# Performance work log

Measured on AMD Instinct MI355X. Metric: run time of the kernel, lower is better.

The kernel has to match this reference:

```python
import jax, jax.numpy as jnp
import numpy as np

B, S, D = 4, 2048, 1024
E, K, H = 8, 2, 1408
LB_WEIGHT = 0.01


def setup_inputs() -> dict:
    key = jax.random.key(0)
    ks = jax.random.split(key, 7)
    sc = 0.02
    return {
        "x": jax.random.normal(ks[0], (B, S, D), dtype=jnp.float32),
        "Wr": jax.random.normal(ks[1], (D, E), dtype=jnp.float32) * sc,
        "Wg": jax.random.normal(ks[2], (E, D, H), dtype=jnp.float32) * sc,
        "Wu": jax.random.normal(ks[3], (E, D, H), dtype=jnp.float32) * sc,
        "Wx": jax.random.normal(ks[4], (E, D, H), dtype=jnp.float32) * sc,
        "Wd": jax.random.normal(ks[5], (E, H, D), dtype=jnp.float32) * sc,
        "alpha": jnp.ones((E,), dtype=jnp.float32),
    }


def _moe(x, Wr, Wg, Wu, Wx, Wd, alpha):
    Bv, Sv, Dv = x.shape
    xf = x.reshape(-1, Dv)  # [T, D]
    router_probs = jax.nn.softmax(xf @ Wr, axis=-1)  # [T, E]
    topk_p, topk_i = jax.lax.top_k(router_probs, K)  # [T, K]
    topk_p = topk_p / jnp.sum(topk_p, axis=-1, keepdims=True)
    # dense combine weights [T, E]; zero for non-selected experts
    combine = jnp.sum(topk_p[..., None] * jax.nn.one_hot(topk_i, E, dtype=xf.dtype), axis=1)
    out = jnp.zeros_like(xf)
    for e in range(E):
        gate = xf @ Wg[e]
        up = xf @ Wu[e]
        expand = xf @ Wx[e]
        ga = jax.nn.silu(gate) * up
        ea = jax.nn.silu(expand) * up
        combined = alpha[e] * ga + (1.0 - alpha[e]) * ea
        eo = combined @ Wd[e]  # [T, D]
        out = out + eo * combine[:, e:e + 1]
    # load balancing loss: mse(mean usage, 1/E)
    usage = jnp.mean(router_probs, axis=0)
    lb = LB_WEIGHT * jnp.mean((usage - 1.0 / E) ** 2)
    return out.reshape(Bv, Sv, Dv), lb


def reference(x, Wr, Wg, Wu, Wx, Wd, alpha):
    return _moe(x, Wr, Wg, Wu, Wx, Wd, alpha)
```

## Files before the change

kernel.cpp:

```cpp
#include <hip/hip_runtime.h>
#include <stdint.h>

typedef unsigned short u16;
typedef __attribute__((ext_vector_type(8))) short short8;
typedef __attribute__((ext_vector_type(4))) float floatx4;

#define T_TOK 8192
#define DM 1024
#define NE 8
#define HD 1408
#define LDA 72

__device__ __forceinline__ float bf2f(u16 u) {
  union { float f; uint32_t i; } v; v.i = ((uint32_t)u) << 16; return v.f;
}
__device__ __forceinline__ u16 f2bf(float f) {
  union { float f; uint32_t i; } v; v.f = f;
  uint32_t r = v.i + 0x7fffu + ((v.i >> 16) & 1u);
  return (u16)(r >> 16);
}
__device__ __forceinline__ floatx4 mfma16(short8 a, short8 b, floatx4 c) {
  return __builtin_amdgcn_mfma_f32_16x16x32_bf16(a, b, c, 0, 0, 0);
}

__global__ void detect_k(const u16* __restrict__ xraw, int* __restrict__ flag) {
  int lane = threadIdx.x & 63;
  u16 w = xraw[lane * 2];
  int ex = (w >> 7) & 0xFF;
  bool hit = (ex >= 100 && ex <= 135);
  unsigned long long m = __ballot(hit);
  if (lane == 0) *flag = (__popcll(m) >= 40) ? 1 : 0;
}

__global__ void conv_alpha_k(const void* __restrict__ araw, u16* __restrict__ ab,
                             const int* __restrict__ flag) {
  int f = *flag;
  if (threadIdx.x < NE) {
    ab[threadIdx.x] = f ? ((const u16*)araw)[threadIdx.x]
                        : f2bf(((const float*)araw)[threadIdx.x]);
  }
}

__global__ __launch_bounds__(256) void conv_x_k(const void* __restrict__ xraw,
                                                u16* __restrict__ xb,
                                                const int* __restrict__ flag) {
  if (*flag) return;
  size_t base = ((size_t)blockIdx.x * 256 + threadIdx.x) * 8;
  const float* s = (const float*)xraw + base;
  float4 v0 = *(const float4*)s;
  float4 v1 = *(const float4*)(s + 4);
  ushort4 o0, o1;
  o0.x = f2bf(v0.x); o0.y = f2bf(v0.y); o0.z = f2bf(v0.z); o0.w = f2bf(v0.w);
  o1.x = f2bf(v1.x); o1.y = f2bf(v1.y); o1.z = f2bf(v1.z); o1.w = f2bf(v1.w);
  *(ushort4*)(xb + base) = o0;
  *(ushort4*)(xb + base + 4) = o1;
}

__global__ __launch_bounds__(256) void transpose_k(
    const void* __restrict__ src, u16* __restrict__ dst, int R, int C,
    const u16* __restrict__ alphab, int mode, const int* __restrict__ flag) {
  int e = blockIdx.z;
  if (mode) {
    float a = bf2f(alphab[e]);
    if (mode == 1 && a == 1.0f) return;
    if (mode == 2 && a == 0.0f) return;
  }
  int f = *flag;
  __shared__ u16 tile[64][65];
  u16* d = dst + (size_t)e * R * C;
  int c0 = blockIdx.x * 64, r0 = blockIdx.y * 64;
  int tx = threadIdx.x & 63, ty = threadIdx.x >> 6;
  if (f) {
    const u16* s = (const u16*)src + (size_t)e * R * C;
    for (int i = ty; i < 64; i += 4)
      tile[i][tx] = s[(size_t)(r0 + i) * C + (c0 + tx)];
  } else {
    const float* s = (const float*)src + (size_t)e * R * C;
    for (int i = ty; i < 64; i += 4)
      tile[i][tx] = f2bf(s[(size_t)(r0 + i) * C + (c0 + tx)]);
  }
  __syncthreads();
  for (int i = ty; i < 64; i += 4)
    d[(size_t)(c0 + i) * R + (r0 + tx)] = tile[tx][i];
}

__global__ __launch_bounds__(256) void rdot_k(
    const void* __restrict__ x, const void* __restrict__ Wr,
    float* __restrict__ probs, const int* __restrict__ flag) {
  int wave = threadIdx.x >> 6, lane = threadIdx.x & 63;
  int t = blockIdx.x * 4 + wave;
  int f = *flag;
  float acc[8];
  #pragma unroll
  for (int e = 0; e < 8; e++) acc[e] = 0.0f;
  if (f) {
    const u16* xr = (const u16*)x + (size_t)t * DM;
    const u16* wr = (const u16*)Wr;
    #pragma unroll
    for (int i = 0; i < 16; i++) {
      int d = i * 64 + lane;
      float xv = bf2f(xr[d]);
      uint4 wv = *(const uint4*)(wr + (size_t)d * 8);
      acc[0] += xv * bf2f((u16)(wv.x & 0xffff));
      acc[1] += xv * bf2f((u16)(wv.x >> 16));
      acc[2] += xv * bf2f((u16)(wv.y & 0xffff));
      acc[3] += xv * bf2f((u16)(wv.y >> 16));
      acc[4] += xv * bf2f((u16)(wv.z & 0xffff));
      acc[5] += xv * bf2f((u16)(wv.z >> 16));
      acc[6] += xv * bf2f((u16)(wv.w & 0xffff));
      acc[7] += xv * bf2f((u16)(wv.w >> 16));
    }
  } else {
    const float* xr = (const float*)x + (size_t)t * DM;
    const float* wr = (const float*)Wr;
    #pragma unroll
    for (int i = 0; i < 16; i++) {
      int d = i * 64 + lane;
      float xv = xr[d];
      float4 w0 = *(const float4*)(wr + (size_t)d * 8);
      float4 w1 = *(const float4*)(wr + (size_t)d * 8 + 4);
      acc[0] += xv * w0.x; acc[1] += xv * w0.y;
      acc[2] += xv * w0.z; acc[3] += xv * w0.w;
      acc[4] += xv * w1.x; acc[5] += xv * w1.y;
      acc[6] += xv * w1.z; acc[7] += xv * w1.w;
    }
  }
  #pragma unroll
  for (int e = 0; e < 8; e++) {
    #pragma unroll
    for (int s = 32; s; s >>= 1) acc[e] += __shfl_xor(acc[e], s, 64);
  }
  float mx = acc[0];
  #pragma unroll
  for (int e = 1; e < 8; e++) mx = fmaxf(mx, acc[e]);
  float p[8], sum = 0.0f;
  #pragma unroll
  for (int e = 0; e < 8; e++) { p[e] = __expf(acc[e] - mx); sum += p[e]; }
  float inv = 1.0f / sum;
  if (lane < 8) probs[(size_t)t * 8 + lane] = p[lane] * inv;
}

__global__ __launch_bounds__(256) void build_k(
    const float* __restrict__ probs, int* __restrict__ counts,
    float* __restrict__ usage, int* __restrict__ tok_ids,
    float* __restrict__ tok_w) {
  __shared__ int sCnt[8];
  __shared__ int sBase[8];
  __shared__ float sUse[8];
  int tid = threadIdx.x;
  if (tid < 8) { sCnt[tid] = 0; sUse[tid] = 0.0f; }
  __syncthreads();

  int t = blockIdx.x * 256 + tid;
  float4 p0 = *(const float4*)(probs + (size_t)t * 8);
  float4 p1 = *(const float4*)(probs + (size_t)t * 8 + 4);
  float p[8] = {p0.x, p0.y, p0.z, p0.w, p1.x, p1.y, p1.z, p1.w};

  #pragma unroll
  for (int e = 0; e < 8; e++) {
    float v = p[e];
    #pragma unroll
    for (int s = 32; s; s >>= 1) v += __shfl_xor(v, s, 64);
    if ((tid & 63) == 0) atomicAdd(&sUse[e], v);
  }

  int e0 = 0;
  #pragma unroll
  for (int e = 1; e < 8; e++) if (p[e] > p[e0]) e0 = e;
  int e1 = (e0 == 0) ? 1 : 0;
  #pragma unroll
  for (int e = 0; e < 8; e++) if (e != e0 && p[e] > p[e1]) e1 = e;
  float s2 = 1.0f / (p[e0] + p[e1]);

  int s0 = atomicAdd(&sCnt[e0], 1);
  int s1 = atomicAdd(&sCnt[e1], 1);
  __syncthreads();
  if (tid < 8) {
    sBase[tid] = atomicAdd(&counts[tid], sCnt[tid]);
    atomicAdd(&usage[tid], sUse[tid]);
  }
  __syncthreads();
  int i0 = sBase[e0] + s0;
  tok_ids[e0 * T_TOK + i0] = t; tok_w[e0 * T_TOK + i0] = p[e0] * s2;
  int i1 = sBase[e1] + s1;
  tok_ids[e1 * T_TOK + i1] = t; tok_w[e1 * T_TOK + i1] = p[e1] * s2;
}

__global__ void scan_k(const int* __restrict__ counts, int* __restrict__ offs) {
  if (threadIdx.x == 0) {
    int s = 0;
    for (int e = 0; e < 8; e++) { offs[e] = s; s += counts[e]; }
    offs[8] = s;
  }
}

__global__ __launch_bounds__(256, 2) void stageA_k(
    const void* __restrict__ xraw, const u16* __restrict__ xb,
    const u16* __restrict__ WgT, const u16* __restrict__ WuT,
    const u16* __restrict__ WxT, const u16* __restrict__ alphab,
    const int* __restrict__ counts, const int* __restrict__ offs,
    const int* __restrict__ tok_ids, u16* __restrict__ comb,
    const int* __restrict__ flag) {
  int e = blockIdx.z;
  int cnt = counts[e];
  int m0 = blockIdx.y * 128;
  if (m0 >= cnt) return;
  int h0 = blockIdx.x * 64;
  int rem = cnt - m0;
  const u16* x = (*flag) ? (const u16*)xraw : xb;

  alignas(16) __shared__ u16 sA[128 * LDA];
  alignas(16) __shared__ u16 sG[64 * LDA];
  alignas(16) __shared__ u16 sU[64 * LDA];
  alignas(16) __shared__ u16 sX[64 * LDA];
  __shared__ int sTok[128];

  int tid = threadIdx.x;
  if (tid < 128)
    sTok[tid] = tok_ids[e * T_TOK + ((tid < rem) ? (m0 + tid) : m0)];
  __syncthreads();

  float aE = bf2f(alphab[e]);
  bool needG = (aE != 0.0f);
  bool needX = (aE != 1.0f);

  const u16* wg = WgT + (size_t)e * HD * DM;
  const u16* wu = WuT + (size_t)e * HD * DM;
  const u16* wx = WxT + (size_t)e * HD * DM;

  int lane = tid & 63, wave = tid >> 6;
  int wm = wave & 1, wn = wave >> 1;
  int lr = lane & 15, quad = lane >> 4;

  int rowA[4], segA[4], rowW[2], segW[2];
  #pragma unroll
  for (int i = 0; i < 4; i++) { int f = tid + 256 * i; rowA[i] = f >> 3; segA[i] = f & 7; }
  #pragma unroll
  for (int i = 0; i < 2; i++) { int f = tid + 256 * i; rowW[i] = f >> 3; segW[i] = f & 7; }

  floatx4 accG[4][2], accU[4][2], accX[4][2];
  #pragma unroll
  for (int i = 0; i < 4; i++)
    #pragma unroll
    for (int j = 0; j < 2; j++) {
      accG[i][j] = (floatx4)0.0f; accU[i][j] = (floatx4)0.0f; accX[i][j] = (floatx4)0.0f;
    }

  short8 rA[4], rU[2], rG[2], rX[2];
  #pragma unroll
  for (int i = 0; i < 4; i++)
    rA[i] = *(const short8*)(x + (size_t)sTok[rowA[i]] * DM + segA[i] * 8);
  #pragma unroll
  for (int i = 0; i < 2; i++) {
    size_t go = (size_t)(h0 + rowW[i]) * DM + segW[i] * 8;
    rU[i] = *(const short8*)(wu + go);
    if (needG) rG[i] = *(const short8*)(wg + go);
    if (needX) rX[i] = *(const short8*)(wx + go);
  }

  const int NK = DM / 64;
  for (int kt = 0; kt < NK; kt++) {
    __syncthreads();
    #pragma unroll
    for (int i = 0; i < 4; i++)
      *(short8*)&sA[rowA[i] * LDA + segA[i] * 8] = rA[i];
    #pragma unroll
    for (int i = 0; i < 2; i++) {
      *(short8*)&sU[rowW[i] * LDA + segW[i] * 8] = rU[i];
      if (needG) *(short8*)&sG[rowW[i] * LDA + segW[i] * 8] = rG[i];
      if (needX) *(short8*)&sX[rowW[i] * LDA + segW[i] * 8] = rX[i];
    }
    __syncthreads();
    if (kt + 1 < NK) {
      int k0 = (kt + 1) * 64;
      #pragma unroll
      for (int i = 0; i < 4; i++)
        rA[i] = *(const short8*)(x + (size_t)sTok[rowA[i]] * DM + k0 + segA[i] * 8);
      #pragma unroll
      for (int i = 0; i < 2; i++) {
        size_t go = (size_t)(h0 + rowW[i]) * DM + k0 + segW[i] * 8;
        rU[i] = *(const short8*)(wu + go);
        if (needG) rG[i] = *(const short8*)(wg + go);
        if (needX) rX[i] = *(const short8*)(wx + go);
      }
    }
    #pragma unroll
    for (int kk = 0; kk < 2; kk++) {
      int kb = kk * 32 + quad * 8;
      short8 a[4];
      #pragma unroll
      for (int i = 0; i < 4; i++)
        a[i] = *(const short8*)&sA[(wm * 64 + i * 16 + lr) * LDA + kb];
      #pragma unroll
      for (int j = 0; j < 2; j++) {
        int nb = (wn * 32 + j * 16 + lr) * LDA + kb;
        short8 bu = *(const short8*)&sU[nb];
        #pragma unroll
        for (int i = 0; i < 4; i++) accU[i][j] = mfma16(a[i], bu, accU[i][j]);
        if (needG) {
          short8 bg = *(const short8*)&sG[nb];
          #pragma unroll
          for (int i = 0; i < 4; i++) accG[i][j] = mfma16(a[i], bg, accG[i][j]);
        }
        if (needX) {
          short8 bx = *(const short8*)&sX[nb];
          #pragma unroll
          for (int i = 0; i < 4; i++) accX[i][j] = mfma16(a[i], bx, accX[i][j]);
        }
      }
    }
  }

  float a1 = aE, a2 = 1.0f - aE;
  size_t rbase = (size_t)(offs[e] + m0);
  #pragma unroll
  for (int i = 0; i < 4; i++) {
    #pragma unroll
    for (int r = 0; r < 4; r++) {
      int row = wm * 64 + i * 16 + quad * 4 + r;
      if (row < rem) {
        u16* cp = comb + (rbase + row) * HD + h0 + wn * 32 + lr;
        #pragma unroll
        for (int j = 0; j < 2; j++) {
          float g = accG[i][j][r], u = accU[i][j][r], xx = accX[i][j][r];
          float sg = g / (1.0f + __expf(-g));
          float sx = xx / (1.0f + __expf(-xx));
          cp[j * 16] = f2bf(u * (a1 * sg + a2 * sx));
        }
      }
    }
  }
}

__global__ __launch_bounds__(256, 2) void stageB_k(
    const u16* __restrict__ comb, const u16* __restrict__ WdT,
    const int* __restrict__ counts, const int* __restrict__ offs,
    const int* __restrict__ tok_ids, const float* __restrict__ tok_w,
    float* __restrict__ accb) {
  int e = blockIdx.z;
  int cnt = counts[e];
  int m0 = blockIdx.y * 128;
  if (m0 >= cnt) return;
  int d0 = blockIdx.x * 128;
  int rem = cnt - m0;

  alignas(16) __shared__ u16 sA[128 * LDA];
  alignas(16) __shared__ u16 sB[128 * LDA];
  __shared__ int sTok[128];
  __shared__ float sW[128];

  int tid = threadIdx.x;
  if (tid < 128) {
    bool v = tid < rem;
    sTok[tid] = v ? tok_ids[e * T_TOK + m0 + tid] : 0;
    sW[tid] = v ? tok_w[e * T_TOK + m0 + tid] : 0.0f;
  }
  __syncthreads();

  const u16* ca = comb + (size_t)(offs[e] + m0) * HD;
  const u16* wd = WdT + (size_t)e * DM * HD;

  int lane = tid & 63, wave = tid >> 6;
  int wm = wave & 1, wn = wave >> 1;
  int lr = lane & 15, quad = lane >> 4;

  int rowS[4], segS[4], rowC[4];
  #pragma unroll
  for (int i = 0; i < 4; i++) {
    int f = tid + 256 * i;
    rowS[i] = f >> 3; segS[i] = f & 7;
    rowC[i] = (rowS[i] < rem) ? rowS[i] : 0;
  }

  floatx4 acc[4][4];
  #pragma unroll
  for (int i = 0; i < 4; i++)
    #pragma unroll
    for (int j = 0; j < 4; j++) acc[i][j] = (floatx4)0.0f;

  short8 rAr[4], rBr[4];
  #pragma unroll
  for (int i = 0; i < 4; i++) {
    rAr[i] = *(const short8*)(ca + (size_t)rowC[i] * HD + segS[i] * 8);
    rBr[i] = *(const short8*)(wd + (size_t)(d0 + rowS[i]) * HD + segS[i] * 8);
  }

  const int NK = HD / 64;
  for (int kt = 0; kt < NK; kt++) {
    __syncthreads();
    #pragma unroll
    for (int i = 0; i < 4; i++) {
      *(short8*)&sA[rowS[i] * LDA + segS[i] * 8] = rAr[i];
      *(short8*)&sB[rowS[i] * LDA + segS[i] * 8] = rBr[i];
    }
    __syncthreads();
    if (kt + 1 < NK) {
      int k0 = (kt + 1) * 64;
      #pragma unroll
      for (int i = 0; i < 4; i++) {
        rAr[i] = *(const short8*)(ca + (size_t)rowC[i] * HD + k0 + segS[i] * 8);
        rBr[i] = *(const short8*)(wd + (size_t)(d0 + rowS[i]) * HD + k0 + segS[i] * 8);
      }
    }
    #pragma unroll
    for (int kk = 0; kk < 2; kk++) {
      int kb = kk * 32 + quad * 8;
      short8 a[4];
      #pragma unroll
      for (int i = 0; i < 4; i++)
        a[i] = *(const short8*)&sA[(wm * 64 + i * 16 + lr) * LDA + kb];
      #pragma unroll
      for (int j = 0; j < 4; j++) {
        short8 b = *(const short8*)&sB[(wn * 64 + j * 16 + lr) * LDA + kb];
        #pragma unroll
        for (int i = 0; i < 4; i++) acc[i][j] = mfma16(a[i], b, acc[i][j]);
      }
    }
  }

  #pragma unroll
  for (int i = 0; i < 4; i++) {
    #pragma unroll
    for (int r = 0; r < 4; r++) {
      int row = wm * 64 + i * 16 + quad * 4 + r;
      if (row < rem) {
        int t = sTok[row];
        float w = sW[row];
        float* orow = accb + (size_t)t * DM + d0 + wn * 64 + lr;
        #pragma unroll
        for (int j = 0; j < 4; j++)
          atomicAdd(&orow[j * 16], acc[i][j][r] * w);
      }
    }
  }
}

__global__ __launch_bounds__(256) void finalize_k(
    const float* __restrict__ accb, const float* __restrict__ usage,
    void* __restrict__ out, const int* __restrict__ flag) {
  int f = *flag;
  size_t idx = (size_t)blockIdx.x * 256 + threadIdx.x;
  float4 v = ((const float4*)accb)[idx];
  float lb = 0.0f;
  if (idx == 0) {
    for (int e = 0; e < 8; e++) {
      float d = usage[e] * (1.0f / 8192.0f) - 0.125f;
      lb += d * d;
    }
    lb *= 0.01f * 0.125f;
  }
  if (f) {
    u16* o = (u16*)out;
    ushort4 ov;
    ov.x = f2bf(v.x); ov.y = f2bf(v.y); ov.z = f2bf(v.z); ov.w = f2bf(v.w);
    ((ushort4*)o)[idx] = ov;
    if (idx == 0) o[(size_t)T_TOK * DM] = f2bf(lb);
  } else {
    float* o = (float*)out;
    ((float4*)o)[idx] = v;
    if (idx == 0) o[(size_t)T_TOK * DM] = lb;
  }
}

extern "C" void kernel_launch(void* const* d_in, const int* in_sizes, int n_in,
                              void* d_out, int out_size, void* d_ws, size_t ws_size,
                              hipStream_t stream) {
  const void* x  = d_in[0];
  const void* Wr = d_in[1];
  const void* Wg = d_in[2];
  const void* Wu = d_in[3];
  const void* Wx = d_in[4];
  const void* Wd = d_in[5];
  const void* al = d_in[6];
  char* ws = (char*)d_ws;

  int*   counts  = (int*)(ws + 0);
  float* usage   = (float*)(ws + 32);
  int*   flag    = (int*)(ws + 64);
  float* accb    = (float*)(ws + 128);
  int*   offs    = (int*)(ws + 33554560);
  int*   tok_ids = (int*)(ws + 33554624);
  float* tok_w   = (float*)(ws + 33816768);
  u16*   alphab  = (u16*)(ws + 34078912);
  u16*   xb      = (u16*)(ws + 34078976);
  u16*   comb    = (u16*)(ws + 50856192);
  u16*   WgT     = (u16*)(ws + 96993536);
  u16*   WuT     = (u16*)(ws + 120062208);
  u16*   WdT     = (u16*)(ws + 143130880);
  float* probs   = (float*)(ws + 166199552);
  u16*   WxT     = (u16*)(ws + 166461696);

  hipMemsetAsync(ws, 0, 33554560, stream);

  dim3 b256(256, 1, 1);
  detect_k<<<dim3(1), dim3(64), 0, stream>>>((const u16*)x, flag);
  conv_alpha_k<<<dim3(1), dim3(64), 0, stream>>>(al, alphab, flag);
  conv_x_k<<<dim3(4096), b256, 0, stream>>>(x, xb, flag);
  transpose_k<<<dim3(HD / 64, DM / 64, NE), b256, 0, stream>>>(Wg, WgT, DM, HD, alphab, 2, flag);
  transpose_k<<<dim3(HD / 64, DM / 64, NE), b256, 0, stream>>>(Wu, WuT, DM, HD, alphab, 0, flag);
  transpose_k<<<dim3(HD / 64, DM / 64, NE), b256, 0, stream>>>(Wx, WxT, DM, HD, alphab, 1, flag);
  transpose_k<<<dim3(DM / 64, HD / 64, NE), b256, 0, stream>>>(Wd, WdT, HD, DM, alphab, 0, flag);
  rdot_k<<<dim3(T_TOK / 4), b256, 0, stream>>>(x, Wr, probs, flag);
  build_k<<<dim3(T_TOK / 256), b256, 0, stream>>>(probs, counts, usage, tok_ids, tok_w);
  scan_k<<<dim3(1), dim3(64), 0, stream>>>(counts, offs);
  stageA_k<<<dim3(HD / 64, T_TOK / 128, NE), b256, 0, stream>>>(
      x, xb, WgT, WuT, WxT, alphab, counts, offs, tok_ids, comb, flag);
  stageB_k<<<dim3(DM / 128, T_TOK / 128, NE), b256, 0, stream>>>(
      comb, WdT, counts, offs, tok_ids, tok_w, accb);
  finalize_k<<<dim3((T_TOK * DM / 4) / 256), b256, 0, stream>>>(accb, usage, d_out, flag);
}
```

Measured before the change: 520.7 us.

## Add alpha==1 specialized stage-A kernel with direct global-to-LDS loads and wider tiles

Adds a stageA2 kernel for experts with alpha==1 that computes only the gate and up GEMMs, using 128x128 tiles and global_load_lds to copy straight into unpadded shared memory. The original stageA now handles only alpha!=1 experts. stageB switches to the same direct LDS loads and drops its register prefetch. The transpose store now writes pairs of u16 values. Direct LDS loads avoid the register round trip but remove the previous prefetch overlap, and the unpadded 64-wide LDS rows may cause bank conflicts on the MFMA operand reads.

```diff
diff --git a/kernel.cpp b/kernel.cpp
--- a/kernel.cpp
+++ b/kernel.cpp
@@ -18,6 +18,10 @@
   union { float f; uint32_t i; } v; v.f = f;
   uint32_t r = v.i + 0x7fffu + ((v.i >> 16) & 1u);
   return (u16)(r >> 16);
+}
+__device__ __forceinline__ void llds16(const void* g, void* l) {
+  __builtin_amdgcn_global_load_lds((const __attribute__((address_space(1))) void*)g,
+                                   (__attribute__((address_space(3))) void*)l, 16, 0, 0);
 }
 __device__ __forceinline__ floatx4 mfma16(short8 a, short8 b, floatx4 c) {
   return __builtin_amdgcn_mfma_f32_16x16x32_bf16(a, b, c, 0, 0, 0);
@@ -80,8 +84,11 @@
       tile[i][tx] = f2bf(s[(size_t)(r0 + i) * C + (c0 + tx)]);
   }
   __syncthreads();
-  for (int i = ty; i < 64; i += 4)
-    d[(size_t)(c0 + i) * R + (r0 + tx)] = tile[tx][i];
+  int i2 = threadIdx.x >> 5, tx2 = threadIdx.x & 31;
+  for (int ii = i2; ii < 64; ii += 8) {
+    ushort2 v; v.x = tile[2 * tx2][ii]; v.y = tile[2 * tx2 + 1][ii];
+    *(ushort2*)&d[(size_t)(c0 + ii) * R + r0 + 2 * tx2] = v;
+  }
 }
 
 __global__ __launch_bounds__(256) void rdot_k(
@@ -194,6 +201,106 @@
   }
 }
 
+__global__ __launch_bounds__(256, 2) void stageA2_k(
+    const void* __restrict__ xraw, const u16* __restrict__ xb,
+    const u16* __restrict__ WgT, const u16* __restrict__ WuT,
+    const u16* __restrict__ alphab, const int* __restrict__ counts,
+    const int* __restrict__ offs, const int* __restrict__ tok_ids,
+    u16* __restrict__ comb, const int* __restrict__ flag) {
+  int e = blockIdx.z;
+  float aE = bf2f(alphab[e]);
+  if (aE != 1.0f) return;
+  int cnt = counts[e];
+  int m0 = blockIdx.y * 128;
+  if (m0 >= cnt) return;
+  int h0 = blockIdx.x * 128;
+  int rem = cnt - m0;
+  const u16* x = (*flag) ? (const u16*)xraw : xb;
+
+  alignas(16) __shared__ u16 sA[128 * 64];
+  alignas(16) __shared__ u16 sG[128 * 64];
+  alignas(16) __shared__ u16 sU[128 * 64];
+  __shared__ int sTok[128];
+
+  int tid = threadIdx.x;
+  if (tid < 128)
+    sTok[tid] = tok_ids[e * T_TOK + ((tid < rem) ? (m0 + tid) : m0)];
+  __syncthreads();
+
+  const u16* wg = WgT + (size_t)e * HD * DM;
+  const u16* wu = WuT + (size_t)e * HD * DM;
+
+  int lane = tid & 63, wave = tid >> 6;
+  int wm = wave & 1, wn = wave >> 1;
+  int lr = lane & 15, quad = lane >> 4;
+
+  const u16* aptr[4]; const u16* gptr[4]; const u16* uptr[4];
+  u16 *dA[4], *dG[4], *dU[4];
+  #pragma unroll
+  for (int i = 0; i < 4; i++) {
+    int f = tid + 256 * i;
+    int row = f >> 3, seg = f & 7;
+    aptr[i] = x + (size_t)sTok[row] * DM + seg * 8;
+    gptr[i] = wg + (size_t)(h0 + row) * DM + seg * 8;
+    uptr[i] = wu + (size_t)(h0 + row) * DM + seg * 8;
+    dA[i] = &sA[f * 8]; dG[i] = &sG[f * 8]; dU[i] = &sU[f * 8];
+  }
+
+  floatx4 accG[4][4], accU[4][4];
+  #pragma unroll
+  for (int i = 0; i < 4; i++)
+    #pragma unroll
+    for (int j = 0; j < 4; j++) { accG[i][j] = (floatx4)0.0f; accU[i][j] = (floatx4)0.0f; }
+
+  for (int kt = 0; kt < DM / 64; kt++) {
+    int k0 = kt * 64;
+    __syncthreads();
+    #pragma unroll
+    for (int i = 0; i < 4; i++) llds16(aptr[i] + k0, dA[i]);
+    #pragma unroll
+    for (int i = 0; i < 4; i++) llds16(uptr[i] + k0, dU[i]);
+    #pragma unroll
+    for (int i = 0; i < 4; i++) llds16(gptr[i] + k0, dG[i]);
+    __syncthreads();
+    #pragma unroll
+    for (int kk = 0; kk < 2; kk++) {
+      int kb = kk * 32 + quad * 8;
+      short8 a[4];
+      #pragma unroll
+      for (int i = 0; i < 4; i++)
+        a[i] = *(const short8*)&sA[(wm * 64 + i * 16 + lr) * 64 + kb];
+      #pragma unroll
+      for (int j = 0; j < 4; j++) {
+        int nb = (wn * 64 + j * 16 + lr) * 64 + kb;
+        short8 bu = *(const short8*)&sU[nb];
+        #pragma unroll
+        for (int i = 0; i < 4; i++) accU[i][j] = mfma16(a[i], bu, accU[i][j]);
+        short8 bg = *(const short8*)&sG[nb];
+        #pragma unroll
+        for (int i = 0; i < 4; i++) accG[i][j] = mfma16(a[i], bg, accG[i][j]);
+      }
+    }
+  }
+
+  size_t rbase = (size_t)(offs[e] + m0);
+  #pragma unroll
+  for (int i = 0; i < 4; i++) {
+    #pragma unroll
+    for (int r = 0; r < 4; r++) {
+      int row = wm * 64 + i * 16 + quad * 4 + r;
+      if (row < rem) {
+        u16* cp = comb + (rbase + row) * HD + h0 + wn * 64 + lr;
+        #pragma unroll
+        for (int j = 0; j < 4; j++) {
+          float g = accG[i][j][r], u = accU[i][j][r];
+          float sg = g / (1.0f + __expf(-g));
+          cp[j * 16] = f2bf(u * sg);
+        }
+      }
+    }
+  }
+}
+
 __global__ __launch_bounds__(256, 2) void stageA_k(
     const void* __restrict__ xraw, const u16* __restrict__ xb,
     const u16* __restrict__ WgT, const u16* __restrict__ WuT,
@@ -202,6 +309,8 @@
     const int* __restrict__ tok_ids, u16* __restrict__ comb,
     const int* __restrict__ flag) {
   int e = blockIdx.z;
+  float aE = bf2f(alphab[e]);
+  if (aE == 1.0f) return;
   int cnt = counts[e];
   int m0 = blockIdx.y * 128;
   if (m0 >= cnt) return;
@@ -220,9 +329,7 @@
     sTok[tid] = tok_ids[e * T_TOK + ((tid < rem) ? (m0 + tid) : m0)];
   __syncthreads();
 
-  float aE = bf2f(alphab[e]);
   bool needG = (aE != 0.0f);
-  bool needX = (aE != 1.0f);
 
   const u16* wg = WgT + (size_t)e * HD * DM;
   const u16* wu = WuT + (size_t)e * HD * DM;
@@ -255,7 +362,7 @@
     size_t go = (size_t)(h0 + rowW[i]) * DM + segW[i] * 8;
     rU[i] = *(const short8*)(wu + go);
     if (needG) rG[i] = *(const short8*)(wg + go);
-    if (needX) rX[i] = *(const short8*)(wx + go);
+    rX[i] = *(const short8*)(wx + go);
   }
 
   const int NK = DM / 64;
@@ -268,7 +375,7 @@
     for (int i = 0; i < 2; i++) {
       *(short8*)&sU[rowW[i] * LDA + segW[i] * 8] = rU[i];
       if (needG) *(short8*)&sG[rowW[i] * LDA + segW[i] * 8] = rG[i];
-      if (needX) *(short8*)&sX[rowW[i] * LDA + segW[i] * 8] = rX[i];
+      *(short8*)&sX[rowW[i] * LDA + segW[i] * 8] = rX[i];
     }
     __syncthreads();
     if (kt + 1 < NK) {
@@ -281,7 +388,7 @@
         size_t go = (size_t)(h0 + rowW[i]) * DM + k0 + segW[i] * 8;
         rU[i] = *(const short8*)(wu + go);
         if (needG) rG[i] = *(const short8*)(wg + go);
-        if (needX) rX[i] = *(const short8*)(wx + go);
+        rX[i] = *(const short8*)(wx + go);
       }
     }
     #pragma unroll
@@ -302,11 +409,9 @@
           #pragma unroll
           for (int i = 0; i < 4; i++) accG[i][j] = mfma16(a[i], bg, accG[i][j]);
         }
-        if (needX) {
-          short8 bx = *(const short8*)&sX[nb];
-          #pragma unroll
-          for (int i = 0; i < 4; i++) accX[i][j] = mfma16(a[i], bx, accX[i][j]);
-        }
+        short8 bx = *(const short8*)&sX[nb];
+        #pragma unroll
+        for (int i = 0; i < 4; i++) accX[i][j] = mfma16(a[i], bx, accX[i][j]);
       }
     }
   }
@@ -344,8 +449,8 @@
   int d0 = blockIdx.x * 128;
   int rem = cnt - m0;
 
-  alignas(16) __shared__ u16 sA[128 * LDA];
-  alignas(16) __shared__ u16 sB[128 * LDA];
+  alignas(16) __shared__ u16 sA[128 * 64];
+  alignas(16) __shared__ u16 sB[128 * 64];
   __shared__ int sTok[128];
   __shared__ float sW[128];
 
@@ -364,12 +469,16 @@
   int wm = wave & 1, wn = wave >> 1;
   int lr = lane & 15, quad = lane >> 4;
 
-  int rowS[4], segS[4], rowC[4];
+  const u16* aptr[4]; const u16* bptr[4];
+  u16 *dA[4], *dB[4];
   #pragma unroll
   for (int i = 0; i < 4; i++) {
     int f = tid + 256 * i;
-    rowS[i] = f >> 3; segS[i] = f & 7;
-    rowC[i] = (rowS[i] < rem) ? rowS[i] : 0;
+    int row = f >> 3, seg = f & 7;
+    int rc = (row < rem) ? row : 0;
+    aptr[i] = ca + (size_t)rc * HD + seg * 8;
+    bptr[i] = wd + (size_t)(d0 + row) * HD + seg * 8;
+    dA[i] = &sA[f * 8]; dB[i] = &sB[f * 8];
   }
 
   floatx4 acc[4][4];
@@ -378,40 +487,24 @@
     #pragma unroll
     for (int j = 0; j < 4; j++) acc[i][j] = (floatx4)0.0f;
 
-  short8 rAr[4], rBr[4];
-  #pragma unroll
-  for (int i = 0; i < 4; i++) {
-    rAr[i] = *(const short8*)(ca + (size_t)rowC[i] * HD + segS[i] * 8);
-    rBr[i] = *(const short8*)(wd + (size_t)(d0 + rowS[i]) * HD + segS[i] * 8);
-  }
-
-  const int NK = HD / 64;
-  for (int kt = 0; kt < NK; kt++) {
+  for (int kt = 0; kt < HD / 64; kt++) {
+    int k0 = kt * 64;
     __syncthreads();
     #pragma unroll
-    for (int i = 0; i < 4; i++) {
-      *(short8*)&sA[rowS[i] * LDA + segS[i] * 8] = rAr[i];
-      *(short8*)&sB[rowS[i] * LDA + segS[i] * 8] = rBr[i];
-    }
+    for (int i = 0; i < 4; i++) llds16(aptr[i] + k0, dA[i]);
+    #pragma unroll
+    for (int i = 0; i < 4; i++) llds16(bptr[i] + k0, dB[i]);
     __syncthreads();
-    if (kt + 1 < NK) {
-      int k0 = (kt + 1) * 64;
-      #pragma unroll
-      for (int i = 0; i < 4; i++) {
-        rAr[i] = *(const short8*)(ca + (size_t)rowC[i] * HD + k0 + segS[i] * 8);
-        rBr[i] = *(const short8*)(wd + (size_t)(d0 + rowS[i]) * HD + k0 + segS[i] * 8);
-      }
-    }
     #pragma unroll
     for (int kk = 0; kk < 2; kk++) {
       int kb = kk * 32 + quad * 8;
       short8 a[4];
       #pragma unroll
       for (int i = 0; i < 4; i++)
-        a[i] = *(const short8*)&sA[(wm * 64 + i * 16 + lr) * LDA + kb];
+        a[i] = *(const short8*)&sA[(wm * 64 + i * 16 + lr) * 64 + kb];
       #pragma unroll
       for (int j = 0; j < 4; j++) {
-        short8 b = *(const short8*)&sB[(wn * 64 + j * 16 + lr) * LDA + kb];
+        short8 b = *(const short8*)&sB[(wn * 64 + j * 16 + lr) * 64 + kb];
         #pragma unroll
         for (int i = 0; i < 4; i++) acc[i][j] = mfma16(a[i], b, acc[i][j]);
       }
@@ -503,6 +596,8 @@
   rdot_k<<<dim3(T_TOK / 4), b256, 0, stream>>>(x, Wr, probs, flag);
   build_k<<<dim3(T_TOK / 256), b256, 0, stream>>>(probs, counts, usage, tok_ids, tok_w);
   scan_k<<<dim3(1), dim3(64), 0, stream>>>(counts, offs);
+  stageA2_k<<<dim3(HD / 128, T_TOK / 128, NE), b256, 0, stream>>>(
+      x, xb, WgT, WuT, alphab, counts, offs, tok_ids, comb, flag);
   stageA_k<<<dim3(HD / 64, T_TOK / 128, NE), b256, 0, stream>>>(
       x, xb, WgT, WuT, WxT, alphab, counts, offs, tok_ids, comb, flag);
   stageB_k<<<dim3(DM / 128, T_TOK / 128, NE), b256, 0, stream>>>(
```

Measured after the change: 508.6 us. 2.3% less time.
